# Kernel optimization log

Measured on AMD Instinct MI355X. Metric: run time of the kernel, lower is better.

The kernel has to match this reference:

```python
import jax, jax.numpy as jnp
import numpy as np

BATCH = 1
SEQ = 3072
HID = 1024
HEADS = 16
HDIM = HID // HEADS  # 64
NSEQ = 8
SLEN = 380
ROPE_BASE = 10.0


def _boundaries():
    b, start = [], 0
    for _ in range(NSEQ):
        b.append((start, start + SLEN))
        start = start + SLEN + 1  # +1 for SEP token
    return b


def setup_inputs() -> dict:
    key = jax.random.key(0)
    ks = jax.random.split(key, 10)
    bnd = _boundaries()
    L = bnd[-1][1]  # actual_length = 3047
    # block-diagonal mask; SEP tokens attend only to themselves
    mask = np.zeros((L, L), dtype=bool)
    for s, e in bnd:
        mask[s:e, s:e] = True
    for s, e in bnd[:-1]:
        mask[e, e] = True
    # position ids reset at each sequence start
    pos = np.zeros((SEQ,), dtype=np.int32)
    for s, e in bnd:
        pos[s:e] = np.arange(e - s, dtype=np.int32)
    sc = 1.0 / np.sqrt(HID)
    return {
        "x": jax.random.normal(ks[0], (BATCH, SEQ, HID), jnp.float32),
        "wq": jax.random.normal(ks[1], (HID, HID), jnp.float32) * sc,
        "bq": jnp.zeros((HID,), jnp.float32),
        "wk": jax.random.normal(ks[2], (HID, HID), jnp.float32) * sc,
        "bk": jnp.zeros((HID,), jnp.float32),
        "wv": jax.random.normal(ks[3], (HID, HID), jnp.float32) * sc,
        "bv": jnp.zeros((HID,), jnp.float32),
        "wo": jax.random.normal(ks[4], (HID, HID), jnp.float32) * sc,
        "bo": jnp.zeros((HID,), jnp.float32),
        "mask": jnp.asarray(mask),
        "position_ids": jnp.asarray(pos)[None, :],  # [1, SEQ]
    }


def _apply_rope(q, k, pos):
    # q, k: [B, S, H, D]; pos: [B, S]
    half = HDIM // 2
    inv_freq = 1.0 / (ROPE_BASE ** (jnp.arange(0, HDIM, 2, dtype=jnp.float32) / HDIM))
    ang = pos.astype(jnp.float32)[..., None] * inv_freq  # [B, S, half]
    cos = jnp.cos(ang)[:, :, None, :]  # [B, S, 1, half]
    sin = jnp.sin(ang)[:, :, None, :]

    def rot(t):
        t1, t2 = t[..., :half], t[..., half:]
        return jnp.concatenate([t1 * cos - t2 * sin, t1 * sin + t2 * cos], axis=-1)

    return rot(q), rot(k)


def reference(x, wq, bq, wk, bk, wv, bv, wo, bo, mask, position_ids):
    B, S, _ = x.shape
    L = mask.shape[0]  # actual_length (static)
    q = (x @ wq.T + bq).reshape(B, S, HEADS, HDIM)
    k = (x @ wk.T + bk).reshape(B, S, HEADS, HDIM)
    v = (x @ wv.T + bv).reshape(B, S, HEADS, HDIM)
    q, k = _apply_rope(q, k, position_ids)
    # [B, H, S, D], trim to packed length
    q = q.transpose(0, 2, 1, 3)[:, :, :L, :]
    k = k.transpose(0, 2, 1, 3)[:, :, :L, :]
    v = v.transpose(0, 2, 1, 3)[:, :, :L, :]
    scores = jnp.einsum("bhqd,bhkd->bhqk", q, k) / jnp.sqrt(jnp.float32(HDIM))
    scores = jnp.where(mask[None, None], scores, -jnp.inf)
    attn = jax.nn.softmax(scores, axis=-1)
    out = jnp.einsum("bhqk,bhkd->bhqd", attn, v)  # [B, H, L, D]
    out = jnp.pad(out, ((0, 0), (0, 0), (0, S - L), (0, 0)))  # zero padded tail
    out = out.transpose(0, 2, 1, 3).reshape(B, S, HID)
    return out @ wo.T + bo
```

## Files before the change

kernel.cpp:

```cpp
#include <hip/hip_runtime.h>

typedef unsigned short u16;
typedef __attribute__((ext_vector_type(8))) short short8;
typedef __attribute__((ext_vector_type(4))) float f32x4;

#define SEQ 3072
#define HID 1024
#define HEADS 16
#define HDIM 64
#define SEGLEN 380
#define SEGSTR 381
#define NSEG 8
#define LTOT 3047
#define VPAD 384

static __device__ __forceinline__ u16 f2bf(float f) {
  unsigned u = __builtin_bit_cast(unsigned, f);
  u += 0x7fffu + ((u >> 16) & 1u);
  return (u16)(u >> 16);
}
static __device__ __forceinline__ float bf2f(u16 h) {
  unsigned u = ((unsigned)h) << 16;
  return __builtin_bit_cast(float, u);
}

static __device__ __forceinline__ void load_lds16(const void* g, void* l) {
  __builtin_amdgcn_global_load_lds((const __attribute__((address_space(1))) void*)g,
                                   (__attribute__((address_space(3))) void*)l, 16, 0, 0);
}

#define BAR() __builtin_amdgcn_s_barrier()
#define VM(N) asm volatile("s_waitcnt vmcnt(" #N ")" ::: "memory")

__global__ void cvt_all_kernel(const float* __restrict__ x, const float* __restrict__ wq,
                               const float* __restrict__ wk, const float* __restrict__ wv,
                               const float* __restrict__ wo, u16* __restrict__ out) {
  const int i = blockIdx.x * 256 + threadIdx.x;
  const float* s;
  int base;
  if (i < 786432)       { s = x;  base = 0; }
  else if (i < 1048576) { s = wq; base = 786432; }
  else if (i < 1310720) { s = wk; base = 1048576; }
  else if (i < 1572864) { s = wv; base = 1310720; }
  else                  { s = wo; base = 1572864; }
  float4 v = reinterpret_cast<const float4*>(s)[i - base];
  unsigned long long o = (unsigned long long)f2bf(v.x) |
                         ((unsigned long long)f2bf(v.y) << 16) |
                         ((unsigned long long)f2bf(v.z) << 32) |
                         ((unsigned long long)f2bf(v.w) << 48);
  reinterpret_cast<unsigned long long*>(out)[i] = o;
}

static __device__ __forceinline__ void stage_qkv(
    const u16* __restrict__ A, const u16* __restrict__ Bw,
    u16* As, u16* Bs, int rowBase, int colBase, int k0) {
  const int tid = threadIdx.x;
  const int w = tid >> 6;
  const int row = tid >> 2;
  const int j = (tid & 3) ^ ((row >> 1) & 3);
  load_lds16(A + (size_t)(rowBase + row) * HID + k0 + j * 8, As + (w * 64) * 8);
  load_lds16(Bw + (size_t)(colBase + row) * HID + k0 + j * 8, Bs + (w * 64) * 8);
}

static __device__ __forceinline__ void compute_qkv(
    const u16* As, const u16* Bs, int wr, int cb0, int lc, int lh, f32x4 (*acc)[2]) {
  short8 af[4], bfv[2];
#pragma unroll
  for (int m = 0; m < 4; ++m) {
    const int row = wr + m * 16 + lc;
    af[m] = *reinterpret_cast<const short8*>(As + row * 32 + (lh ^ ((row >> 1) & 3)) * 8);
  }
#pragma unroll
  for (int n = 0; n < 2; ++n) {
    const int row = cb0 + n * 32 + lc;
    bfv[n] = *reinterpret_cast<const short8*>(Bs + row * 32 + (lh ^ ((row >> 1) & 3)) * 8);
  }
  __builtin_amdgcn_s_setprio(1);
#pragma unroll
  for (int m = 0; m < 4; ++m)
#pragma unroll
    for (int n = 0; n < 2; ++n)
      acc[m][n] = __builtin_amdgcn_mfma_f32_16x16x32_bf16(af[m], bfv[n], acc[m][n], 0, 0, 0);
  __builtin_amdgcn_s_setprio(0);
}

__global__ __launch_bounds__(512) void qkv_gemm_kernel(
    const u16* __restrict__ xb,
    const u16* __restrict__ wqb, const u16* __restrict__ wkb, const u16* __restrict__ wvb,
    const float* __restrict__ bq, const float* __restrict__ bk, const float* __restrict__ bv,
    u16* __restrict__ qb, u16* __restrict__ kbuf, u16* __restrict__ vT) {
  __shared__ u16 As[3][128 * 32];
  __shared__ u16 Bs[3][128 * 32];
  const int which = blockIdx.y >> 3;
  const u16* Bw = (which == 0) ? wqb : (which == 1) ? wkb : wvb;
  const float* bias = (which == 0) ? bq : (which == 1) ? bk : bv;
  const int rowBase = blockIdx.x * 128;
  const int colBase = (blockIdx.y & 7) * 128;
  const int tid = threadIdx.x;
  const int w = tid >> 6, l = tid & 63, lc = l & 15, lh = l >> 4;
  const int wr = (w >> 2) * 64;
  const int c2 = w & 3;
  const int cb0 = (c2 >> 1) * 64 + (c2 & 1) * 16;

  f32x4 acc[4][2];
  f32x4 z4 = {0.f, 0.f, 0.f, 0.f};
#pragma unroll
  for (int m = 0; m < 4; ++m) { acc[m][0] = z4; acc[m][1] = z4; }

  stage_qkv(xb, Bw, As[0], Bs[0], rowBase, colBase, 0);
  stage_qkv(xb, Bw, As[1], Bs[1], rowBase, colBase, 32);
#pragma unroll 1
  for (int t = 0; t < 30; t += 3) {
    stage_qkv(xb, Bw, As[2], Bs[2], rowBase, colBase, (t + 2) * 32);
    VM(4); BAR();
    compute_qkv(As[0], Bs[0], wr, cb0, lc, lh, acc);
    BAR();
    stage_qkv(xb, Bw, As[0], Bs[0], rowBase, colBase, (t + 3) * 32);
    VM(4); BAR();
    compute_qkv(As[1], Bs[1], wr, cb0, lc, lh, acc);
    BAR();
    stage_qkv(xb, Bw, As[1], Bs[1], rowBase, colBase, (t + 4) * 32);
    VM(4); BAR();
    compute_qkv(As[2], Bs[2], wr, cb0, lc, lh, acc);
    BAR();
  }
  VM(2); BAR();
  compute_qkv(As[0], Bs[0], wr, cb0, lc, lh, acc);
  BAR();
  VM(0); BAR();
  compute_qkv(As[1], Bs[1], wr, cb0, lc, lh, acc);

  const int f = (c2 & 1) * 16 + lc;
  const int col0 = colBase + (c2 >> 1) * 64 + f;
  if (which < 2) {
    u16* outp = which ? kbuf : qb;
    const float bv0 = bias[col0];
    const float bv1 = bias[col0 + 32];
    const float invf = exp2f(-(float)f * 0.10381025296523007f);
#pragma unroll
    for (int m = 0; m < 4; ++m) {
      const int row0 = rowBase + wr + m * 16 + lh * 4;
#pragma unroll
      for (int r = 0; r < 4; ++r) {
        const int row = row0 + r;
        const int rr = row % SEGSTR;
        const float pos = (float)((rr < SEGLEN) ? rr : 0);
        float sn, cs;
        sincosf(pos * invf, &sn, &cs);
        const float t1 = acc[m][0][r] + bv0;
        const float t2 = acc[m][1][r] + bv1;
        const size_t base = (size_t)row * HID + col0;
        outp[base] = f2bf(t1 * cs - t2 * sn);
        outp[base + 32] = f2bf(t1 * sn + t2 * cs);
      }
    }
  } else {
#pragma unroll
    for (int n = 0; n < 2; ++n) {
      const int col = col0 + n * 32;
      const float bvl = bias[col];
#pragma unroll
      for (int m = 0; m < 4; ++m) {
        const int row0 = rowBase + wr + m * 16 + lh * 4;
#pragma unroll
        for (int r = 0; r < 4; ++r) {
          const float v = acc[m][n][r] + bvl;
          const int row = row0 + r;
          const int sg = row / SEGSTR;
          const int j = row - sg * SEGSTR;
          if (sg < NSEG)
            vT[(size_t)col * (NSEG * VPAD) + sg * VPAD + j] = f2bf(v);
        }
      }
    }
  }
}

static __device__ __forceinline__ void stage_out(
    const u16* __restrict__ A, const u16* __restrict__ Bw,
    u16* As, u16* Bs, int rowBase, int colBase, int k0) {
  const int tid = threadIdx.x;
  const int w = tid >> 6;
#pragma unroll
  for (int c = 0; c < 2; ++c) {
    const int li = c * 512 + tid;
    const int row = li >> 3;
    const int j = (li & 7) ^ (row & 7);
    load_lds16(A + (size_t)(rowBase + row) * HID + k0 + j * 8,
               As + (c * 512 + w * 64) * 8);
  }
  {
    const int row = tid >> 3;
    const int j = (tid & 7) ^ (row & 7);
    load_lds16(Bw + (size_t)(colBase + row) * HID + k0 + j * 8, Bs + (w * 64) * 8);
  }
}

static __device__ __forceinline__ void compute_out(
    const u16* As, const u16* Bs, int wrO, int wcO, int lc, int lh, f32x4 (*acc)[2]) {
  short8 af[2][2], bfv[2][2];
#pragma unroll
  for (int m = 0; m < 2; ++m) {
    const int row = wrO + m * 16 + lc;
#pragma unroll
    for (int ks = 0; ks < 2; ++ks)
      af[m][ks] = *reinterpret_cast<const short8*>(
          As + row * 64 + (((ks * 4 + lh) ^ (row & 7))) * 8);
  }
#pragma unroll
  for (int n = 0; n < 2; ++n) {
    const int row = wcO + n * 16 + lc;
#pragma unroll
    for (int ks = 0; ks < 2; ++ks)
      bfv[n][ks] = *reinterpret_cast<const short8*>(
          Bs + row * 64 + (((ks * 4 + lh) ^ (row & 7))) * 8);
  }
  __builtin_amdgcn_s_setprio(1);
#pragma unroll
  for (int ks = 0; ks < 2; ++ks)
#pragma unroll
    for (int m = 0; m < 2; ++m)
#pragma unroll
      for (int n = 0; n < 2; ++n)
        acc[m][n] = __builtin_amdgcn_mfma_f32_16x16x32_bf16(af[m][ks], bfv[n][ks], acc[m][n], 0, 0, 0);
  __builtin_amdgcn_s_setprio(0);
}

__global__ __launch_bounds__(512) void out_gemm_kernel(
    const u16* __restrict__ aob, const u16* __restrict__ wob,
    const float* __restrict__ bo, float* __restrict__ out) {
  __shared__ u16 As[3][128 * 64];
  __shared__ u16 Bs[3][64 * 64];
  const int rowBase = blockIdx.x * 128;
  const int colBase = blockIdx.y * 64;
  const int tid = threadIdx.x;
  const int w = tid >> 6, l = tid & 63, lc = l & 15, lh = l >> 4;
  const int wrO = (w >> 1) * 32, wcO = (w & 1) * 32;
  f32x4 acc[2][2];
  f32x4 z4 = {0.f, 0.f, 0.f, 0.f};
#pragma unroll
  for (int m = 0; m < 2; ++m) { acc[m][0] = z4; acc[m][1] = z4; }

  stage_out(aob, wob, As[0], Bs[0], rowBase, colBase, 0);
  stage_out(aob, wob, As[1], Bs[1], rowBase, colBase, 64);
#pragma unroll 1
  for (int t = 0; t < 12; t += 3) {
    stage_out(aob, wob, As[2], Bs[2], rowBase, colBase, (t + 2) * 64);
    VM(6); BAR();
    compute_out(As[0], Bs[0], wrO, wcO, lc, lh, acc);
    BAR();
    stage_out(aob, wob, As[0], Bs[0], rowBase, colBase, (t + 3) * 64);
    VM(6); BAR();
    compute_out(As[1], Bs[1], wrO, wcO, lc, lh, acc);
    BAR();
    stage_out(aob, wob, As[1], Bs[1], rowBase, colBase, (t + 4) * 64);
    VM(6); BAR();
    compute_out(As[2], Bs[2], wrO, wcO, lc, lh, acc);
    BAR();
  }
  stage_out(aob, wob, As[2], Bs[2], rowBase, colBase, 14 * 64);
  VM(6); BAR();
  compute_out(As[0], Bs[0], wrO, wcO, lc, lh, acc);
  BAR();
  stage_out(aob, wob, As[0], Bs[0], rowBase, colBase, 15 * 64);
  VM(6); BAR();
  compute_out(As[1], Bs[1], wrO, wcO, lc, lh, acc);
  BAR();
  VM(3); BAR();
  compute_out(As[2], Bs[2], wrO, wcO, lc, lh, acc);
  BAR();
  VM(0); BAR();
  compute_out(As[0], Bs[0], wrO, wcO, lc, lh, acc);

#pragma unroll
  for (int n = 0; n < 2; ++n) {
    const int col = colBase + wcO + n * 16 + lc;
    const float bvl = bo[col];
#pragma unroll
    for (int m = 0; m < 2; ++m) {
      const int row0 = rowBase + wrO + m * 16 + lh * 4;
#pragma unroll
      for (int r = 0; r < 4; ++r)
        out[(size_t)(row0 + r) * HID + col] = acc[m][n][r] + bvl;
    }
  }
}

__global__ __launch_bounds__(256) void attn_kernel(
    const u16* __restrict__ qb, const u16* __restrict__ kb,
    const u16* __restrict__ vT, u16* __restrict__ ao) {
  __shared__ u16 Ks[3][32 * 64];
  __shared__ u16 Vs[3][64 * 32];
  __shared__ u16 P_lds[4][16 * 32];
  const int tid = threadIdx.x;
  const int w = tid >> 6, l = tid & 63, lc = l & 15, lh = l >> 4;
  const int W = (blockIdx.x & 7) * 96 + (blockIdx.x >> 3);
  const int qt = W % 6;
  const int seg = (W / 6) & 7;
  const int h = W / 48;
  const int segbase = seg * SEGSTR;
  const int rloc = qt * 64 + w * 16;

  const u16* qrow = qb + (size_t)(segbase + rloc + lc) * HID + h * HDIM + lh * 8;
  const short8 qf0 = *reinterpret_cast<const short8*>(qrow);
  const short8 qf1 = *reinterpret_cast<const short8*>(qrow + 32);

  const size_t vstride = (size_t)NSEG * VPAD;
  const u16* kseg = kb + (size_t)segbase * HID + h * HDIM;
  const u16* vseg = vT + (size_t)h * HDIM * vstride + seg * VPAD;

  const int krow = tid >> 3;
  const int kj = (tid & 7) ^ (krow & 7);
  const int vd = tid >> 2;
  const int vj = (tid & 3) ^ ((vd >> 2) & 3);

  f32x4 z4 = {0.f, 0.f, 0.f, 0.f};
  f32x4 accO[4] = {z4, z4, z4, z4};
  float psum[4] = {0.f, 0.f, 0.f, 0.f};

  u16* pl = &P_lds[w][0];
  int wo0[4], wo1[4];
#pragma unroll
  for (int r = 0; r < 4; ++r) {
    const int prow = lh * 4 + r;
    const int sw = (prow >> 1) & 3;
    wo0[r] = prow * 32 + ((lc >> 3) ^ sw) * 8 + (lc & 7);
    wo1[r] = prow * 32 + ((2 + (lc >> 3)) ^ sw) * 8 + (lc & 7);
  }
  const int prd_off = lc * 32 + (lh ^ ((lc >> 1) & 3)) * 8;

#define STAGE(B, T)                                                                 \
  load_lds16(kseg + (size_t)((T) * 32 + krow) * HID + kj * 8, &Ks[B][0] + w * 512); \
  load_lds16(vseg + (size_t)vd * vstride + (T) * 32 + vj * 8, &Vs[B][0] + w * 512);

#define STEP(B, MASKED)                                                               \
  {                                                                                   \
    const u16* KB = &Ks[B][0];                                                        \
    const u16* VB = &Vs[B][0];                                                        \
    const int ks0 = (lh ^ (lc & 7)) * 8;                                              \
    const int ks1 = ((lh + 4) ^ (lc & 7)) * 8;                                        \
    const short8 k00 = *reinterpret_cast<const short8*>(KB + lc * 64 + ks0);          \
    const short8 k01 = *reinterpret_cast<const short8*>(KB + lc * 64 + ks1);          \
    const short8 k10 = *reinterpret_cast<const short8*>(KB + (16 + lc) * 64 + ks0);   \
    const short8 k11 = *reinterpret_cast<const short8*>(KB + (16 + lc) * 64 + ks1);   \
    f32x4 s0 = z4, s1 = z4;                                                           \
    __builtin_amdgcn_s_setprio(1);                                                    \
    s0 = __builtin_amdgcn_mfma_f32_16x16x32_bf16(qf0, k00, s0, 0, 0, 0);              \
    s0 = __builtin_amdgcn_mfma_f32_16x16x32_bf16(qf1, k01, s0, 0, 0, 0);              \
    s1 = __builtin_amdgcn_mfma_f32_16x16x32_bf16(qf0, k10, s1, 0, 0, 0);              \
    s1 = __builtin_amdgcn_mfma_f32_16x16x32_bf16(qf1, k11, s1, 0, 0, 0);              \
    __builtin_amdgcn_s_setprio(0);                                                    \
    float p0[4], p1[4];                                                               \
    _Pragma("unroll") for (int r = 0; r < 4; ++r) {                                   \
      p0[r] = (!(MASKED) || lc < 28) ? __expf(s0[r] * 0.125f) : 0.f;                  \
      p1[r] = (!(MASKED) || lc < 12) ? __expf(s1[r] * 0.125f) : 0.f;                  \
      psum[r] += p0[r] + p1[r];                                                       \
    }                                                                                 \
    _Pragma("unroll") for (int r = 0; r < 4; ++r) {                                   \
      pl[wo0[r]] = f2bf(p0[r]);                                                       \
      pl[wo1[r]] = f2bf(p1[r]);                                                       \
    }                                                                                 \
    const short8 pf = *reinterpret_cast<const short8*>(pl + prd_off);                 \
    const int vsw = (lh ^ (lc >> 2)) * 8;                                             \
    const short8 v0 = *reinterpret_cast<const short8*>(VB + lc * 32 + vsw);           \
    const short8 v1 = *reinterpret_cast<const short8*>(VB + (16 + lc) * 32 + vsw);    \
    const short8 v2 = *reinterpret_cast<const short8*>(VB + (32 + lc) * 32 + vsw);    \
    const short8 v3 = *reinterpret_cast<const short8*>(VB + (48 + lc) * 32 + vsw);    \
    __builtin_amdgcn_s_setprio(1);                                                    \
    accO[0] = __builtin_amdgcn_mfma_f32_16x16x32_bf16(pf, v0, accO[0], 0, 0, 0);      \
    accO[1] = __builtin_amdgcn_mfma_f32_16x16x32_bf16(pf, v1, accO[1], 0, 0, 0);      \
    accO[2] = __builtin_amdgcn_mfma_f32_16x16x32_bf16(pf, v2, accO[2], 0, 0, 0);      \
    accO[3] = __builtin_amdgcn_mfma_f32_16x16x32_bf16(pf, v3, accO[3], 0, 0, 0);      \
    __builtin_amdgcn_s_setprio(0);                                                    \
  }

  STAGE(0, 0);
  STAGE(1, 1);
#pragma unroll 1
  for (int t = 0; t < 9; t += 3) {
    STAGE(2, t + 2);
    VM(4); BAR();
    STEP(0, false);
    BAR();
    STAGE(0, t + 3);
    VM(4); BAR();
    STEP(1, false);
    BAR();
    STAGE(1, t + 4);
    VM(4); BAR();
    STEP(2, false);
    BAR();
  }
  STAGE(2, 11);
  VM(4); BAR();
  STEP(0, false);
  BAR();
  VM(2); BAR();
  STEP(1, false);
  BAR();
  VM(0); BAR();
  STEP(2, true);
#undef STEP
#undef STAGE

  float inv[4];
#pragma unroll
  for (int r = 0; r < 4; ++r) {
    float s = psum[r];
    s += __shfl_xor(s, 1);
    s += __shfl_xor(s, 2);
    s += __shfl_xor(s, 4);
    s += __shfl_xor(s, 8);
    inv[r] = 1.0f / s;
  }
#pragma unroll
  for (int r = 0; r < 4; ++r) {
    const int lrow = rloc + lh * 4 + r;
    if (lrow < SEGLEN) {
      const size_t orow = (size_t)(segbase + lrow) * HID + h * HDIM;
#pragma unroll
      for (int n = 0; n < 4; ++n)
        ao[orow + n * 16 + lc] = f2bf(accO[n][r] * inv[r]);
    }
  }

  if (qt == 5) {
    if (seg < NSEG - 1) {
      if (tid < HDIM)
        ao[(size_t)(segbase + SEGLEN) * HID + h * HDIM + tid] =
            vT[(size_t)(h * HDIM + tid) * vstride + seg * VPAD + SEGLEN];
    } else {
#pragma unroll
      for (int k = 0; k < 7; ++k) {
        const int idx = k * 256 + tid;
        if (idx < 25 * HDIM) {
          const int rr = idx >> 6, cc = idx & 63;
          ao[(size_t)(LTOT + rr) * HID + h * HDIM + cc] = 0;
        }
      }
    }
  }
}

extern "C" void kernel_launch(void* const* d_in, const int* in_sizes, int n_in,
                              void* d_out, int out_size, void* d_ws, size_t ws_size,
                              hipStream_t stream) {
  const float* x  = (const float*)d_in[0];
  const float* wq = (const float*)d_in[1];
  const float* bq = (const float*)d_in[2];
  const float* wk = (const float*)d_in[3];
  const float* bk = (const float*)d_in[4];
  const float* wv = (const float*)d_in[5];
  const float* bv = (const float*)d_in[6];
  const float* wo = (const float*)d_in[7];
  const float* bo = (const float*)d_in[8];
  float* out = (float*)d_out;

  u16* ws = (u16*)d_ws;
  u16* xb   = ws;
  u16* wqb  = xb  + (size_t)SEQ * HID;
  u16* wkb  = wqb + (size_t)HID * HID;
  u16* wvb  = wkb + (size_t)HID * HID;
  u16* wob  = wvb + (size_t)HID * HID;
  u16* qb   = wob + (size_t)HID * HID;
  u16* kbuf = qb  + (size_t)SEQ * HID;
  u16* vT   = kbuf + (size_t)SEQ * HID;
  u16* aob  = vT  + (size_t)HID * (NSEG * VPAD);

  cvt_all_kernel<<<7168, 256, 0, stream>>>(x, wq, wk, wv, wo, ws);

  qkv_gemm_kernel<<<dim3(SEQ / 128, 24), 512, 0, stream>>>(
      xb, wqb, wkb, wvb, bq, bk, bv, qb, kbuf, vT);

  attn_kernel<<<768, 256, 0, stream>>>(qb, kbuf, vT, aob);

  out_gemm_kernel<<<dim3(SEQ / 128, HID / 64), 512, 0, stream>>>(aob, wob, bo, out);

  (void)in_sizes; (void)n_in; (void)out_size; (void)ws_size;
}
```

Before: 79.71 us.

## Warp-specialize QKV GEMM with dedicated producer wave for LDS staging

Adds a ninth wave to the QKV GEMM block that alone issues all global-to-LDS loads across the triple-buffered pipeline. The eight compute waves now only run MFMA work, synchronised with the producer by matching barrier sequences. The aim is to take load issue and vmcnt waits off the compute waves' critical path. In exchange, one wave must issue 16 loads per stage, which may bottleneck staging, and the block grows to 576 threads, which can affect occupancy.

Result: slower. 84.20 us (+5.6%).

```diff
diff --git a/kernel.cpp b/kernel.cpp
--- a/kernel.cpp
+++ b/kernel.cpp
@@ -30,6 +30,7 @@
 }
 
 #define BAR() __builtin_amdgcn_s_barrier()
+#define FENCE() asm volatile("" ::: "memory")
 #define VM(N) asm volatile("s_waitcnt vmcnt(" #N ")" ::: "memory")
 
 __global__ void cvt_all_kernel(const float* __restrict__ x, const float* __restrict__ wq,
@@ -51,15 +52,15 @@
   reinterpret_cast<unsigned long long*>(out)[i] = o;
 }
 
-static __device__ __forceinline__ void stage_qkv(
-    const u16* __restrict__ A, const u16* __restrict__ Bw,
-    u16* As, u16* Bs, int rowBase, int colBase, int k0) {
-  const int tid = threadIdx.x;
-  const int w = tid >> 6;
-  const int row = tid >> 2;
-  const int j = (tid & 3) ^ ((row >> 1) & 3);
-  load_lds16(A + (size_t)(rowBase + row) * HID + k0 + j * 8, As + (w * 64) * 8);
-  load_lds16(Bw + (size_t)(colBase + row) * HID + k0 + j * 8, Bs + (w * 64) * 8);
+static __device__ __forceinline__ void pstage_mat(
+    const u16* __restrict__ src, u16* dst, int base, int k0, int lane) {
+#pragma unroll
+  for (int i = 0; i < 8; ++i) {
+    const int ci = i * 64 + lane;
+    const int row = ci >> 2;
+    const int j = (ci & 3) ^ ((row >> 1) & 3);
+    load_lds16(src + (size_t)(base + row) * HID + k0 + j * 8, dst + i * 512);
+  }
 }
 
 static __device__ __forceinline__ void compute_qkv(
@@ -84,7 +85,7 @@
   __builtin_amdgcn_s_setprio(0);
 }
 
-__global__ __launch_bounds__(512) void qkv_gemm_kernel(
+__global__ __launch_bounds__(576) void qkv_gemm_kernel(
     const u16* __restrict__ xb,
     const u16* __restrict__ wqb, const u16* __restrict__ wkb, const u16* __restrict__ wvb,
     const float* __restrict__ bq, const float* __restrict__ bk, const float* __restrict__ bv,
@@ -98,6 +99,26 @@
   const int colBase = (blockIdx.y & 7) * 128;
   const int tid = threadIdx.x;
   const int w = tid >> 6, l = tid & 63, lc = l & 15, lh = l >> 4;
+
+  if (w == 8) {
+    const int lane = l;
+#define PSTG(BUF, T)                                        \
+  pstage_mat(xb, &As[BUF][0], rowBase, (T) * 32, lane);     \
+  pstage_mat(Bw, &Bs[BUF][0], colBase, (T) * 32, lane);
+    PSTG(0, 0);
+    PSTG(1, 1);
+    VM(16); BAR(); FENCE();
+#pragma unroll 1
+    for (int t = 0; t < 30; t += 3) {
+      PSTG(2, t + 2); VM(16); BAR(); FENCE();
+      PSTG(0, t + 3); VM(16); BAR(); FENCE();
+      PSTG(1, t + 4); VM(16); BAR(); FENCE();
+    }
+    VM(0); BAR(); FENCE();
+#undef PSTG
+    return;
+  }
+
   const int wr = (w >> 2) * 64;
   const int c2 = w & 3;
   const int cb0 = (c2 >> 1) * 64 + (c2 & 1) * 16;
@@ -107,27 +128,18 @@
 #pragma unroll
   for (int m = 0; m < 4; ++m) { acc[m][0] = z4; acc[m][1] = z4; }
 
-  stage_qkv(xb, Bw, As[0], Bs[0], rowBase, colBase, 0);
-  stage_qkv(xb, Bw, As[1], Bs[1], rowBase, colBase, 32);
+  BAR(); FENCE();
 #pragma unroll 1
   for (int t = 0; t < 30; t += 3) {
-    stage_qkv(xb, Bw, As[2], Bs[2], rowBase, colBase, (t + 2) * 32);
-    VM(4); BAR();
     compute_qkv(As[0], Bs[0], wr, cb0, lc, lh, acc);
-    BAR();
-    stage_qkv(xb, Bw, As[0], Bs[0], rowBase, colBase, (t + 3) * 32);
-    VM(4); BAR();
+    BAR(); FENCE();
     compute_qkv(As[1], Bs[1], wr, cb0, lc, lh, acc);
-    BAR();
-    stage_qkv(xb, Bw, As[1], Bs[1], rowBase, colBase, (t + 4) * 32);
-    VM(4); BAR();
+    BAR(); FENCE();
     compute_qkv(As[2], Bs[2], wr, cb0, lc, lh, acc);
-    BAR();
-  }
-  VM(2); BAR();
+    BAR(); FENCE();
+  }
   compute_qkv(As[0], Bs[0], wr, cb0, lc, lh, acc);
-  BAR();
-  VM(0); BAR();
+  BAR(); FENCE();
   compute_qkv(As[1], Bs[1], wr, cb0, lc, lh, acc);
 
   const int f = (c2 & 1) * 16 + lc;
@@ -469,7 +481,7 @@
 
   cvt_all_kernel<<<7168, 256, 0, stream>>>(x, wq, wk, wv, wo, ws);
 
-  qkv_gemm_kernel<<<dim3(SEQ / 128, 24), 512, 0, stream>>>(
+  qkv_gemm_kernel<<<dim3(SEQ / 128, 24), 576, 0, stream>>>(
       xb, wqb, wkb, wvb, bq, bk, bv, qb, kbuf, vT);
 
   attn_kernel<<<768, 256, 0, stream>>>(qb, kbuf, vT, aob);
```

## Pre-tile and swizzle x and QKV weights into contiguous GEMM blocks during conversion

Applied to the files above, without the earlier changes.

The fp32-to-bf16 conversion now writes x and the Q/K/V weights in a tile-blocked, pre-swizzled layout, so each 128x32 K-slice of a GEMM tile is one contiguous 8KB chunk. The QKV GEMM staging then loads fully contiguous 16-byte chunks instead of strided rows. Each conversion thread also handles 8 elements instead of 4, halving the grid. The cost is scattered 32-byte reads in the conversion kernel, in exchange for better-coalesced GEMM loads.

After: 74.33 us. 1.07x faster.

```diff
diff --git a/kernel.cpp b/kernel.cpp
--- a/kernel.cpp
+++ b/kernel.cpp
@@ -34,32 +34,49 @@
 
 __global__ void cvt_all_kernel(const float* __restrict__ x, const float* __restrict__ wq,
                                const float* __restrict__ wk, const float* __restrict__ wv,
-                               const float* __restrict__ wo, u16* __restrict__ out) {
-  const int i = blockIdx.x * 256 + threadIdx.x;
-  const float* s;
-  int base;
-  if (i < 786432)       { s = x;  base = 0; }
-  else if (i < 1048576) { s = wq; base = 786432; }
-  else if (i < 1310720) { s = wk; base = 1048576; }
-  else if (i < 1572864) { s = wv; base = 1310720; }
-  else                  { s = wo; base = 1572864; }
-  float4 v = reinterpret_cast<const float4*>(s)[i - base];
-  unsigned long long o = (unsigned long long)f2bf(v.x) |
-                         ((unsigned long long)f2bf(v.y) << 16) |
-                         ((unsigned long long)f2bf(v.z) << 32) |
-                         ((unsigned long long)f2bf(v.w) << 48);
-  reinterpret_cast<unsigned long long*>(out)[i] = o;
+                               const float* __restrict__ wo, u16* __restrict__ ws) {
+  const int d = blockIdx.x * 256 + threadIdx.x;
+  const float* src;
+  if (d < 393216) {
+    const int tm = d >> 14, rem = d & 16383;
+    const int tk = rem >> 9, rem2 = rem & 511;
+    const int row = rem2 >> 2, cp = rem2 & 3;
+    const int j = cp ^ ((row >> 1) & 3);
+    src = x + ((size_t)(tm * 128 + row) * HID + tk * 32 + j * 8);
+  } else if (d < 786432) {
+    const int dd = d - 393216;
+    const int tc = dd >> 14, rem = dd & 16383;
+    const int tk = rem >> 9, rem2 = rem & 511;
+    const int row = rem2 >> 2, cp = rem2 & 3;
+    const int j = cp ^ ((row >> 1) & 3);
+    const int which = tc >> 3;
+    const float* wsrc = (which == 0) ? wq : (which == 1) ? wk : wv;
+    src = wsrc + ((size_t)((tc & 7) * 128 + row) * HID + tk * 32 + j * 8);
+  } else {
+    src = wo + (size_t)(d - 786432) * 8;
+  }
+  float4 a = *reinterpret_cast<const float4*>(src);
+  float4 b = *reinterpret_cast<const float4*>(src + 4);
+  unsigned long long o0 = (unsigned long long)f2bf(a.x) |
+                          ((unsigned long long)f2bf(a.y) << 16) |
+                          ((unsigned long long)f2bf(a.z) << 32) |
+                          ((unsigned long long)f2bf(a.w) << 48);
+  unsigned long long o1 = (unsigned long long)f2bf(b.x) |
+                          ((unsigned long long)f2bf(b.y) << 16) |
+                          ((unsigned long long)f2bf(b.z) << 32) |
+                          ((unsigned long long)f2bf(b.w) << 48);
+  unsigned long long* dst = reinterpret_cast<unsigned long long*>(ws + (size_t)d * 8);
+  dst[0] = o0;
+  dst[1] = o1;
 }
 
 static __device__ __forceinline__ void stage_qkv(
-    const u16* __restrict__ A, const u16* __restrict__ Bw,
-    u16* As, u16* Bs, int rowBase, int colBase, int k0) {
+    const u16* __restrict__ Ablk, const u16* __restrict__ Bblk,
+    u16* As, u16* Bs, int t) {
   const int tid = threadIdx.x;
   const int w = tid >> 6;
-  const int row = tid >> 2;
-  const int j = (tid & 3) ^ ((row >> 1) & 3);
-  load_lds16(A + (size_t)(rowBase + row) * HID + k0 + j * 8, As + (w * 64) * 8);
-  load_lds16(Bw + (size_t)(colBase + row) * HID + k0 + j * 8, Bs + (w * 64) * 8);
+  load_lds16(Ablk + (size_t)t * 4096 + tid * 8, As + (w * 64) * 8);
+  load_lds16(Bblk + (size_t)t * 4096 + tid * 8, Bs + (w * 64) * 8);
 }
 
 static __device__ __forceinline__ void compute_qkv(
@@ -85,17 +102,17 @@
 }
 
 __global__ __launch_bounds__(512) void qkv_gemm_kernel(
-    const u16* __restrict__ xb,
-    const u16* __restrict__ wqb, const u16* __restrict__ wkb, const u16* __restrict__ wvb,
+    const u16* __restrict__ xblk, const u16* __restrict__ wblk,
     const float* __restrict__ bq, const float* __restrict__ bk, const float* __restrict__ bv,
     u16* __restrict__ qb, u16* __restrict__ kbuf, u16* __restrict__ vT) {
   __shared__ u16 As[3][128 * 32];
   __shared__ u16 Bs[3][128 * 32];
   const int which = blockIdx.y >> 3;
-  const u16* Bw = (which == 0) ? wqb : (which == 1) ? wkb : wvb;
   const float* bias = (which == 0) ? bq : (which == 1) ? bk : bv;
   const int rowBase = blockIdx.x * 128;
   const int colBase = (blockIdx.y & 7) * 128;
+  const u16* Ablk = xblk + (size_t)blockIdx.x * 131072;
+  const u16* Bblk = wblk + (size_t)blockIdx.y * 131072;
   const int tid = threadIdx.x;
   const int w = tid >> 6, l = tid & 63, lc = l & 15, lh = l >> 4;
   const int wr = (w >> 2) * 64;
@@ -107,19 +124,19 @@
 #pragma unroll
   for (int m = 0; m < 4; ++m) { acc[m][0] = z4; acc[m][1] = z4; }
 
-  stage_qkv(xb, Bw, As[0], Bs[0], rowBase, colBase, 0);
-  stage_qkv(xb, Bw, As[1], Bs[1], rowBase, colBase, 32);
+  stage_qkv(Ablk, Bblk, As[0], Bs[0], 0);
+  stage_qkv(Ablk, Bblk, As[1], Bs[1], 1);
 #pragma unroll 1
   for (int t = 0; t < 30; t += 3) {
-    stage_qkv(xb, Bw, As[2], Bs[2], rowBase, colBase, (t + 2) * 32);
+    stage_qkv(Ablk, Bblk, As[2], Bs[2], t + 2);
     VM(4); BAR();
     compute_qkv(As[0], Bs[0], wr, cb0, lc, lh, acc);
     BAR();
-    stage_qkv(xb, Bw, As[0], Bs[0], rowBase, colBase, (t + 3) * 32);
+    stage_qkv(Ablk, Bblk, As[0], Bs[0], t + 3);
     VM(4); BAR();
     compute_qkv(As[1], Bs[1], wr, cb0, lc, lh, acc);
     BAR();
-    stage_qkv(xb, Bw, As[1], Bs[1], rowBase, colBase, (t + 4) * 32);
+    stage_qkv(Ablk, Bblk, As[1], Bs[1], t + 4);
     VM(4); BAR();
     compute_qkv(As[2], Bs[2], wr, cb0, lc, lh, acc);
     BAR();
@@ -457,20 +474,18 @@
   float* out = (float*)d_out;
 
   u16* ws = (u16*)d_ws;
-  u16* xb   = ws;
-  u16* wqb  = xb  + (size_t)SEQ * HID;
-  u16* wkb  = wqb + (size_t)HID * HID;
-  u16* wvb  = wkb + (size_t)HID * HID;
-  u16* wob  = wvb + (size_t)HID * HID;
+  u16* xblk = ws;
+  u16* wblk = xblk + (size_t)SEQ * HID;
+  u16* wob  = wblk + (size_t)3 * HID * HID;
   u16* qb   = wob + (size_t)HID * HID;
   u16* kbuf = qb  + (size_t)SEQ * HID;
   u16* vT   = kbuf + (size_t)SEQ * HID;
   u16* aob  = vT  + (size_t)HID * (NSEG * VPAD);
 
-  cvt_all_kernel<<<7168, 256, 0, stream>>>(x, wq, wk, wv, wo, ws);
+  cvt_all_kernel<<<3584, 256, 0, stream>>>(x, wq, wk, wv, wo, ws);
 
   qkv_gemm_kernel<<<dim3(SEQ / 128, 24), 512, 0, stream>>>(
-      xb, wqb, wkb, wvb, bq, bk, bv, qb, kbuf, vT);
+      xblk, wblk, bq, bk, bv, qb, kbuf, vT);
 
   attn_kernel<<<768, 256, 0, stream>>>(qb, kbuf, vT, aob);
 
```
